# Optimization experiments

Hardware: AMD Instinct MI355X
Metric: run time of the kernel (lower is better)

## Reference

```python
import jax, jax.numpy as jnp
import numpy as np


def setup_inputs() -> dict:
    key = jax.random.key(0)
    ks = jax.random.split(key, 8)
    B, L, D = 8, 4096, 1024
    s = 1.0 / np.sqrt(D)  # torch Linear default init scale (approx)
    return {
        "x": jax.random.normal(ks[0], (B, L, D), dtype=jnp.float32),
        "hidden": jax.random.normal(ks[1], (B, D), dtype=jnp.float32),
        "W_f": jax.random.normal(ks[2], (D, D), dtype=jnp.float32) * s,
        "b_f": jnp.zeros((D,), dtype=jnp.float32),
        "W_i": jax.random.normal(ks[3], (D, D), dtype=jnp.float32) * s,
        "b_i": jnp.zeros((D,), dtype=jnp.float32),
        "W_o": jax.random.normal(ks[4], (D, D), dtype=jnp.float32) * s,
        "b_o": jnp.zeros((D,), dtype=jnp.float32),
    }


def reference(x, hidden, W_f, b_f, W_i, b_i, W_o, b_o):
    # x: [B, L, D], hidden: [B, D]
    D = x.shape[-1]
    lin = jnp.linspace(0.0, 1.0, D, dtype=x.dtype)  # per-channel gate scale
    remember = jax.nn.sigmoid(jnp.einsum('bld,ed->ble', x, W_f) + b_f) * lin
    forget = 1.0 - remember
    inp = jnp.tanh(jnp.einsum('bld,ed->ble', x, W_i) + b_i) * remember

    # linear recurrence h_t = forget_t * h_{t-1} + inp_t  via parallel scan
    def combine(c1, c2):
        a1, u1 = c1
        a2, u2 = c2
        return (a1 * a2, a2 * u1 + u2)

    cumprod_forget, h_inner = jax.lax.associative_scan(combine, (forget, inp), axis=1)
    h = h_inner + hidden[:, None, :] * cumprod_forget  # inject initial hidden state
    y = jnp.einsum('bld,ed->ble', h, W_o) + b_o
    return y, h
```

## Files before the change

### kernel.cpp

```cpp
#include <hip/hip_runtime.h>
#include <stdint.h>

#define B_ 8
#define L_ 4096
#define D_ 1024
#define M_ (B_*L_)
#define CHUNKS 128
#define TCH (L_/CHUNKS)

typedef float f32x4 __attribute__((ext_vector_type(4)));
typedef float f32x2 __attribute__((ext_vector_type(2)));
typedef short short8 __attribute__((ext_vector_type(8)));
typedef unsigned short ushort4v __attribute__((ext_vector_type(4)));

static __device__ __forceinline__ unsigned short f2bf(float f) {
  union { float f; unsigned u; } v; v.f = f;
  unsigned r = v.u + 0x7FFFu + ((v.u >> 16) & 1u);
  return (unsigned short)(r >> 16);
}
static __device__ __forceinline__ float bf2f(unsigned short u) {
  union { unsigned u; float f; } v; v.u = ((unsigned)u) << 16; return v.f;
}

#define GLOAD16(g, l) \
  __builtin_amdgcn_global_load_lds((__attribute__((address_space(1))) const void*)(g), \
                                   (__attribute__((address_space(3))) void*)(l), 16, 0, 0)

__global__ __launch_bounds__(256)
void cvt_bf16(const float* __restrict__ src, unsigned short* __restrict__ dst, int n8)
{
  int gid = blockIdx.x * 256 + threadIdx.x;
  if (gid >= n8) return;
  const f32x4* s = (const f32x4*)(src + (size_t)gid * 8);
  f32x4 v0 = s[0], v1 = s[1];
  union { short8 v; unsigned short u[8]; } w;
  w.u[0] = f2bf(v0[0]); w.u[1] = f2bf(v0[1]); w.u[2] = f2bf(v0[2]); w.u[3] = f2bf(v0[3]);
  w.u[4] = f2bf(v1[0]); w.u[5] = f2bf(v1[1]); w.u[6] = f2bf(v1[2]); w.u[7] = f2bf(v1[3]);
  *(short8*)(dst + (size_t)gid * 8) = w.v;
}

__global__ __launch_bounds__(256)
void cvt_w3(const float* __restrict__ w0, const float* __restrict__ w1,
            const float* __restrict__ w2, unsigned short* __restrict__ dst)
{
  const int per = (D_ * D_) / 8 / 256;
  int m = blockIdx.x / per;
  int gid = (blockIdx.x % per) * 256 + threadIdx.x;
  const float* src = (m == 0) ? w0 : (m == 1) ? w1 : w2;
  const f32x4* s = (const f32x4*)(src + (size_t)gid * 8);
  f32x4 v0 = s[0], v1 = s[1];
  union { short8 v; unsigned short u[8]; } w;
  w.u[0] = f2bf(v0[0]); w.u[1] = f2bf(v0[1]); w.u[2] = f2bf(v0[2]); w.u[3] = f2bf(v0[3]);
  w.u[4] = f2bf(v1[0]); w.u[5] = f2bf(v1[1]); w.u[6] = f2bf(v1[2]); w.u[7] = f2bf(v1[3]);
  *(short8*)(dst + (size_t)m * D_ * D_ + (size_t)gid * 8) = w.v;
}

template<int MODE>
__global__ __launch_bounds__(512, 2)
void gemm256(const unsigned short* __restrict__ A,
             const unsigned short* __restrict__ Bw,
             const float* __restrict__ bias0,
             const float* __restrict__ bias1,
             unsigned short* __restrict__ ob0,
             unsigned short* __restrict__ ob1,
             float* __restrict__ of)
{
  __shared__ unsigned short lds[65536];
  char* ldsb = (char*)lds;

  const int tid  = threadIdx.x;
  const int lane = tid & 63;
  const int wid  = tid >> 6;
  const int wm   = wid >> 2;
  const int wn   = wid & 3;
  const int frow = lane & 15, ks = lane >> 4;
  const int xsw  = (ks ^ ((frow >> 1) & 3)) << 4;

  constexpr int NBN = (MODE == 0) ? 8 : 4;
  constexpr int GBM = 32 / NBN;
  const int xcd   = blockIdx.x & 7;
  const int slot  = blockIdx.x >> 3;
  const int local = slot & 31;
  const int wrnd  = slot >> 5;
  const int bm = (xcd * 16 + wrnd * GBM + (local & (GBM - 1))) * 256;
  const int bn = (local / GBM) * 256;

  const int r0  = tid >> 2;
  const int scl = ((tid & 3) ^ ((r0 >> 1) & 3)) << 4;
  const char* pA = (const char*)A  + (size_t)(bm + r0) * 2048 + scl;
  const char* pB = (const char*)Bw + (size_t)(bn + r0) * 2048 + scl;
  const int dst16 = tid * 16;

  f32x4 acc[8][4] = {};
  short8 aq[4], bq[4];

  auto stgA = [&](int T, int kk, int buf) {
    const char* s = pA + T * 128 + kk * 64;
    char* d = ldsb + buf * 32768 + kk * 16384 + dst16;
    GLOAD16(s, d);
    GLOAD16(s + (size_t)128 * 2048, d + 8192);
  };
  auto stgB = [&](int T, int kk, int buf) {
    const char* s = pB + T * 128 + kk * 64;
    char* d = ldsb + 65536 + buf * 32768 + kk * 16384 + dst16;
    GLOAD16(s, d);
    GLOAD16(s + (size_t)128 * 2048, d + 8192);
  };
  auto ldA4 = [&](const char* LA, int kk, int ih) {
    const char* base = LA + kk * 16384 + (wm * 128 + ih * 64 + frow) * 64 + xsw;
    aq[0] = *(const short8*)(base);
    aq[1] = *(const short8*)(base + 1024);
    aq[2] = *(const short8*)(base + 2048);
    aq[3] = *(const short8*)(base + 3072);
  };
  auto ldB4 = [&](const char* LB, int kk) {
    const char* base = LB + kk * 16384 + (wn * 64 + frow) * 64 + xsw;
    bq[0] = *(const short8*)(base);
    bq[1] = *(const short8*)(base + 1024);
    bq[2] = *(const short8*)(base + 2048);
    bq[3] = *(const short8*)(base + 3072);
  };
  auto mfma16 = [&](int ih) {
    __builtin_amdgcn_s_setprio(1);
    #pragma unroll
    for (int i2 = 0; i2 < 4; ++i2) {
      #pragma unroll
      for (int j = 0; j < 4; ++j)
        acc[ih * 4 + i2][j] =
          __builtin_amdgcn_mfma_f32_16x16x32_bf16(aq[i2], bq[j], acc[ih * 4 + i2][j], 0, 0, 0);
    }
    __builtin_amdgcn_s_setprio(0);
  };

  stgA(0, 0, 0); stgB(0, 0, 0);
  stgA(0, 1, 0); stgB(0, 1, 0);
  stgA(1, 0, 1); stgB(1, 0, 1);
  asm volatile("s_waitcnt vmcnt(8)" ::: "memory");
  __builtin_amdgcn_s_barrier();

  for (int t = 0; t < 16; ++t) {
    const int buf = t & 1;
    const char* LA = ldsb + buf * 32768;
    const char* LB = ldsb + 65536 + buf * 32768;
    ldB4(LB, 0);
    ldA4(LA, 0, 0);
    if (t < 15) stgA(t + 1, 1, (t + 1) & 1);
    __builtin_amdgcn_s_barrier();
    asm volatile("s_waitcnt lgkmcnt(0)" ::: "memory");
    mfma16(0);
    __builtin_amdgcn_s_barrier();
    ldA4(LA, 0, 1);
    if (t < 15) stgB(t + 1, 1, (t + 1) & 1);
    if (t < 15) asm volatile("s_waitcnt vmcnt(8)" ::: "memory");
    else        asm volatile("s_waitcnt vmcnt(0)" ::: "memory");
    __builtin_amdgcn_s_barrier();
    asm volatile("s_waitcnt lgkmcnt(0)" ::: "memory");
    mfma16(1);
    __builtin_amdgcn_s_barrier();
    ldB4(LB, 1);
    ldA4(LA, 1, 0);
    if (t < 14) stgA(t + 2, 0, buf);
    __builtin_amdgcn_s_barrier();
    asm volatile("s_waitcnt lgkmcnt(0)" ::: "memory");
    mfma16(0);
    __builtin_amdgcn_s_barrier();
    ldA4(LA, 1, 1);
    if (t < 14) stgB(t + 2, 0, buf);
    if (t < 14) asm volatile("s_waitcnt vmcnt(8)" ::: "memory");
    else        asm volatile("s_waitcnt vmcnt(4)" ::: "memory");
    __builtin_amdgcn_s_barrier();
    asm volatile("s_waitcnt lgkmcnt(0)" ::: "memory");
    mfma16(1);
    __builtin_amdgcn_s_barrier();
  }

  if constexpr (MODE == 0) {
    const int plane = bn >> 10;
    const int cb    = bn & 1023;
    unsigned short* ob = plane ? ob1 : ob0;
    const float* bs    = plane ? bias1 : bias0;
    float bv[4];
    #pragma unroll
    for (int j = 0; j < 4; ++j) bv[j] = bs[cb + wn * 64 + j * 16 + frow];
    #pragma unroll
    for (int ii = 0; ii < 8; ++ii) {
      int row = bm + wm * 128 + ii * 16 + ks * 4;
      #pragma unroll
      for (int j = 0; j < 4; ++j) {
        int col = cb + wn * 64 + j * 16 + frow;
        #pragma unroll
        for (int r = 0; r < 4; ++r)
          ob[(size_t)(row + r) * D_ + col] = f2bf(acc[ii][j][r] + bv[j]);
      }
    }
  } else {
    float bv[4];
    #pragma unroll
    for (int j = 0; j < 4; ++j) bv[j] = bias0[bn + wn * 64 + j * 16 + frow];
    #pragma unroll
    for (int ii = 0; ii < 8; ++ii) {
      int row = bm + wm * 128 + ii * 16 + ks * 4;
      #pragma unroll
      for (int j = 0; j < 4; ++j) {
        int col = bn + wn * 64 + j * 16 + frow;
        #pragma unroll
        for (int r = 0; r < 4; ++r)
          of[(size_t)(row + r) * D_ + col] = acc[ii][j][r] + bv[j];
      }
    }
  }
}

static __device__ __forceinline__ void gate1(float zf, float zi, float lin,
                                             float& f, float& inp)
{
  float rem = lin / (1.0f + __expf(-zf));
  float ez  = __expf(2.0f * zi);
  float th  = 1.0f - 2.0f / (ez + 1.0f);
  f = 1.0f - rem;
  inp = th * rem;
}

__global__ __launch_bounds__(256)
void scan_partial_b(const unsigned short* __restrict__ zf,
                    const unsigned short* __restrict__ zi,
                    float* __restrict__ Ag, float* __restrict__ Ug)
{
  int blk = blockIdx.x;
  int b = blk >> 7, c = blk & (CHUNKS - 1);
  int e = threadIdx.x << 2;
  float lin0 = (float)e * (1.0f / 1023.0f);
  size_t base = ((size_t)b * L_ + (size_t)c * TCH) * D_ + e;
  f32x4 a = {1.f,1.f,1.f,1.f}, u = {0.f,0.f,0.f,0.f};
  for (int t = 0; t < TCH; ++t) {
    ushort4v f4 = *(const ushort4v*)(zf + base + (size_t)t * D_);
    ushort4v i4 = *(const ushort4v*)(zi + base + (size_t)t * D_);
    #pragma unroll
    for (int j = 0; j < 4; ++j) {
      float fg, inp;
      gate1(bf2f(f4[j]), bf2f(i4[j]), lin0 + (float)j * (1.0f/1023.0f), fg, inp);
      u[j] = fmaf(fg, u[j], inp);
      a[j] *= fg;
    }
  }
  size_t o = (size_t)(b * CHUNKS + c) * D_ + e;
  *(f32x4*)(Ag + o) = a;
  *(f32x4*)(Ug + o) = u;
}

__global__ __launch_bounds__(256)
void scan_carry(const float* __restrict__ Ag, const float* __restrict__ Ug,
                const float* __restrict__ hidden, float* __restrict__ Hin)
{
  int gid = blockIdx.x * 256 + threadIdx.x;
  int b = gid >> 8;
  int e = (gid & 255) << 2;
  f32x4 h = *(const f32x4*)(hidden + (size_t)b * D_ + e);
  for (int c = 0; c < CHUNKS; ++c) {
    size_t o = (size_t)(b * CHUNKS + c) * D_ + e;
    *(f32x4*)(Hin + o) = h;
    f32x4 A = *(const f32x4*)(Ag + o);
    f32x4 U = *(const f32x4*)(Ug + o);
    h = A * h + U;
  }
}

__global__ __launch_bounds__(256)
void scan_apply_b(const unsigned short* __restrict__ zf,
                  const unsigned short* __restrict__ zi,
                  const float* __restrict__ Hin,
                  float* __restrict__ hout, unsigned short* __restrict__ hb)
{
  int blk = blockIdx.x;
  int b = blk >> 7, c = blk & (CHUNKS - 1);
  int e = threadIdx.x << 2;
  float lin0 = (float)e * (1.0f / 1023.0f);
  size_t base = ((size_t)b * L_ + (size_t)c * TCH) * D_ + e;
  f32x4 h = *(const f32x4*)(Hin + (size_t)(b * CHUNKS + c) * D_ + e);
  for (int t = 0; t < TCH; ++t) {
    size_t o = base + (size_t)t * D_;
    ushort4v f4 = *(const ushort4v*)(zf + o);
    ushort4v i4 = *(const ushort4v*)(zi + o);
    #pragma unroll
    for (int j = 0; j < 4; ++j) {
      float fg, inp;
      gate1(bf2f(f4[j]), bf2f(i4[j]), lin0 + (float)j * (1.0f/1023.0f), fg, inp);
      h[j] = fmaf(fg, h[j], inp);
    }
    *(f32x4*)(hout + o) = h;
    ushort4v p;
    p[0] = f2bf(h[0]); p[1] = f2bf(h[1]); p[2] = f2bf(h[2]); p[3] = f2bf(h[3]);
    *(ushort4v*)(hb + o) = p;
  }
}

template<int MODE>
__global__ __launch_bounds__(256, 2)
void gemm_slow(const float* __restrict__ A, const float* __restrict__ B0,
               const float* __restrict__ B1, const float* __restrict__ bias0,
               const float* __restrict__ bias1, float* __restrict__ out0,
               float* __restrict__ out1)
{
  constexpr int BK = 32;
  __shared__ unsigned short As[128 * BK];
  __shared__ unsigned short Bs0[128 * BK];
  __shared__ unsigned short Bs1[(MODE == 0) ? (128 * BK) : 8];

  const int tid = threadIdx.x, lane = tid & 63, wave = tid >> 6;
  const int wr = wave >> 1, wc = wave & 1;
  const int bm = blockIdx.x * 128, bn = blockIdx.y * 128;
  f32x4 acc0[4][4] = {};
  f32x4 acc1[(MODE == 0) ? 4 : 1][(MODE == 0) ? 4 : 1] = {};
  const int frow = lane & 15, kslot = lane >> 4;
  const int xs = kslot ^ (frow & 3);

  auto stage = [&](const float* src, unsigned short* dst) {
    #pragma unroll
    for (int p = 0; p < 4; ++p) {
      int g = p * 256 + tid;
      int row = g >> 3, kq = (g & 7) << 2;
      f32x4 v = *(const f32x4*)(src + (size_t)row * D_ + kq);
      ushort4v w;
      w[0] = f2bf(v[0]); w[1] = f2bf(v[1]); w[2] = f2bf(v[2]); w[3] = f2bf(v[3]);
      int byte = kq << 1, slot = byte >> 4, sub = byte & 15;
      int off = row * 64 + ((slot ^ (row & 3)) << 4) + sub;
      *(ushort4v*)((char*)dst + off) = w;
    }
  };

  for (int k0 = 0; k0 < D_; k0 += BK) {
    stage(A + (size_t)bm * D_ + k0, As);
    stage(B0 + (size_t)bn * D_ + k0, Bs0);
    if constexpr (MODE == 0) stage(B1 + (size_t)bn * D_ + k0, Bs1);
    __syncthreads();
    short8 af[4], bf0[4], bf1[4];
    #pragma unroll
    for (int i = 0; i < 4; ++i) {
      int ar = wr * 64 + i * 16 + frow;
      af[i] = *(const short8*)((const char*)As + ar * 64 + (xs << 4));
      int br = wc * 64 + i * 16 + frow;
      bf0[i] = *(const short8*)((const char*)Bs0 + br * 64 + (xs << 4));
      if constexpr (MODE == 0)
        bf1[i] = *(const short8*)((const char*)Bs1 + br * 64 + (xs << 4));
    }
    #pragma unroll
    for (int i = 0; i < 4; ++i)
      #pragma unroll
      for (int j = 0; j < 4; ++j) {
        acc0[i][j] = __builtin_amdgcn_mfma_f32_16x16x32_bf16(af[i], bf0[j], acc0[i][j], 0, 0, 0);
        if constexpr (MODE == 0)
          acc1[i][j] = __builtin_amdgcn_mfma_f32_16x16x32_bf16(af[i], bf1[j], acc1[i][j], 0, 0, 0);
      }
    __syncthreads();
  }
  #pragma unroll
  for (int i = 0; i < 4; ++i)
    #pragma unroll
    for (int j = 0; j < 4; ++j)
      #pragma unroll
      for (int r = 0; r < 4; ++r) {
        int row = bm + wr * 64 + i * 16 + (lane >> 4) * 4 + r;
        int col = bn + wc * 64 + j * 16 + (lane & 15);
        size_t idx = (size_t)row * D_ + col;
        if constexpr (MODE == 0) {
          float zf = acc0[i][j][r] + bias0[col];
          float linv = (float)col * (1.0f / 1023.0f);
          float rem = linv / (1.0f + __expf(-zf));
          float zi = acc1[i][j][r] + bias1[col];
          float e2 = __expf(2.0f * zi);
          float th = 1.0f - 2.0f / (e2 + 1.0f);
          out0[idx] = 1.0f - rem;
          out1[idx] = th * rem;
        } else {
          out0[idx] = acc0[i][j][r] + bias0[col];
        }
      }
}

__global__ __launch_bounds__(256)
void scan_partial_f(const float* __restrict__ p0, const float* __restrict__ p1,
                    float* __restrict__ Ag, float* __restrict__ Ug)
{
  int blk = blockIdx.x;
  int b = blk / (CHUNKS * 2);
  int c = (blk >> 1) & (CHUNKS - 1);
  int e = ((blk & 1) << 9) + threadIdx.x * 2;
  size_t base = ((size_t)b * L_ + (size_t)c * TCH) * D_ + e;
  f32x2 a = {1.0f, 1.0f}, u = {0.0f, 0.0f};
  for (int t = 0; t < TCH; ++t) {
    f32x2 f = *(const f32x2*)(p0 + base + (size_t)t * D_);
    f32x2 i = *(const f32x2*)(p1 + base + (size_t)t * D_);
    u = f * u + i;
    a = a * f;
  }
  size_t o = (size_t)(b * CHUNKS + c) * D_ + e;
  *(f32x2*)(Ag + o) = a;
  *(f32x2*)(Ug + o) = u;
}

__global__ __launch_bounds__(256)
void scan_apply_f(const float* __restrict__ p0, float* __restrict__ p1_io,
                  const float* __restrict__ Hin)
{
  int blk = blockIdx.x;
  int b = blk / (CHUNKS * 2);
  int c = (blk >> 1) & (CHUNKS - 1);
  int e = ((blk & 1) << 9) + threadIdx.x * 2;
  size_t base = ((size_t)b * L_ + (size_t)c * TCH) * D_ + e;
  f32x2 h = *(const f32x2*)(Hin + (size_t)(b * CHUNKS + c) * D_ + e);
  for (int t = 0; t < TCH; ++t) {
    size_t o = base + (size_t)t * D_;
    f32x2 f = *(const f32x2*)(p0 + o);
    f32x2 i = *(const f32x2*)(p1_io + o);
    h = f * h + i;
    *(f32x2*)(p1_io + o) = h;
  }
}

extern "C" void kernel_launch(void* const* d_in, const int* in_sizes, int n_in,
                              void* d_out, int out_size, void* d_ws, size_t ws_size,
                              hipStream_t stream)
{
  const float* x      = (const float*)d_in[0];
  const float* hidden = (const float*)d_in[1];
  const float* W_f    = (const float*)d_in[2];
  const float* b_f    = (const float*)d_in[3];
  const float* W_i    = (const float*)d_in[4];
  const float* b_i    = (const float*)d_in[5];
  const float* W_o    = (const float*)d_in[6];
  const float* b_o    = (const float*)d_in[7];

  float* y = (float*)d_out;
  float* h = y + (size_t)M_ * D_;

  const size_t xb_elems = (size_t)M_ * D_;
  const size_t w_elems  = (size_t)D_ * D_;
  const size_t agg      = (size_t)B_ * CHUNKS * D_;
  const size_t need = (xb_elems * 3 + 3 * w_elems) * 2 + agg * 3 * 4;

  if (ws_size >= need) {
    unsigned short* xb  = (unsigned short*)d_ws;
    unsigned short* wfb = xb + xb_elems;
    unsigned short* wib = wfb + w_elems;
    unsigned short* wob = wib + w_elems;
    unsigned short* zfb = wob + w_elems;
    unsigned short* zib = zfb + xb_elems;
    float* Ag  = (float*)(zib + xb_elems);
    float* Ug  = Ag + agg;
    float* Hin = Ug + agg;

    cvt_bf16<<<(int)(xb_elems / 8 / 256), 256, 0, stream>>>(x, xb, (int)(xb_elems / 8));
    cvt_w3<<<3 * (int)(w_elems / 8 / 256), 256, 0, stream>>>(W_f, W_i, W_o, wfb);

    gemm256<0><<<1024, 512, 0, stream>>>(xb, wfb, b_f, b_i, zfb, zib, nullptr);

    int pblocks = B_ * CHUNKS;
    scan_partial_b<<<pblocks, 256, 0, stream>>>(zfb, zib, Ag, Ug);
    scan_carry<<<(B_ * D_ / 4) / 256, 256, 0, stream>>>(Ag, Ug, hidden, Hin);
    scan_apply_b<<<pblocks, 256, 0, stream>>>(zfb, zib, Hin, h, xb);

    gemm256<1><<<512, 512, 0, stream>>>(xb, wob, b_o, nullptr, nullptr, nullptr, y);
  } else {
    float* Ag  = (float*)d_ws;
    float* Ug  = Ag + agg;
    float* Hin = Ug + agg;
    dim3 gg(M_ / 128, D_ / 128);
    int pblocks = B_ * CHUNKS * 2;

    gemm_slow<0><<<gg, 256, 0, stream>>>(x, W_f, W_i, b_f, b_i, y, h);
    scan_partial_f<<<pblocks, 256, 0, stream>>>(y, h, Ag, Ug);
    scan_carry<<<(B_ * D_ / 4) / 256, 256, 0, stream>>>(Ag, Ug, hidden, Hin);
    scan_apply_f<<<pblocks, 256, 0, stream>>>(y, h, Hin);
    gemm_slow<1><<<gg, 256, 0, stream>>>(h, W_o, nullptr, b_o, nullptr, y, nullptr);
  }
}
```

Measured before the change: 390.9 us.

## Fuse gate activations into GEMM epilogue and hand-unroll pipelined K loop

```diff
diff --git a/kernel.cpp b/kernel.cpp
--- a/kernel.cpp
+++ b/kernel.cpp
@@ -106,19 +106,24 @@
     GLOAD16(s, d);
     GLOAD16(s + (size_t)128 * 2048, d + 8192);
   };
+  auto ldAB4 = [&](const char* LA, const char* LB, int kk, int ih) {
+    const char* ab = LA + kk * 16384 + (wm * 128 + ih * 64 + frow) * 64 + xsw;
+    const char* bb = LB + kk * 16384 + (wn * 64 + frow) * 64 + xsw;
+    aq[0] = *(const short8*)(ab);
+    bq[0] = *(const short8*)(bb);
+    bq[1] = *(const short8*)(bb + 1024);
+    bq[2] = *(const short8*)(bb + 2048);
+    bq[3] = *(const short8*)(bb + 3072);
+    aq[1] = *(const short8*)(ab + 1024);
+    aq[2] = *(const short8*)(ab + 2048);
+    aq[3] = *(const short8*)(ab + 3072);
+  };
   auto ldA4 = [&](const char* LA, int kk, int ih) {
-    const char* base = LA + kk * 16384 + (wm * 128 + ih * 64 + frow) * 64 + xsw;
-    aq[0] = *(const short8*)(base);
-    aq[1] = *(const short8*)(base + 1024);
-    aq[2] = *(const short8*)(base + 2048);
-    aq[3] = *(const short8*)(base + 3072);
-  };
-  auto ldB4 = [&](const char* LB, int kk) {
-    const char* base = LB + kk * 16384 + (wn * 64 + frow) * 64 + xsw;
-    bq[0] = *(const short8*)(base);
-    bq[1] = *(const short8*)(base + 1024);
-    bq[2] = *(const short8*)(base + 2048);
-    bq[3] = *(const short8*)(base + 3072);
+    const char* ab = LA + kk * 16384 + (wm * 128 + ih * 64 + frow) * 64 + xsw;
+    aq[0] = *(const short8*)(ab);
+    aq[1] = *(const short8*)(ab + 1024);
+    aq[2] = *(const short8*)(ab + 2048);
+    aq[3] = *(const short8*)(ab + 3072);
   };
   auto mfma16 = [&](int ih) {
     __builtin_amdgcn_s_setprio(1);
@@ -132,47 +137,48 @@
     __builtin_amdgcn_s_setprio(0);
   };
 
+#define DO_TILE(T, BUF, STG1, STG2, W1, W3)                                   \
+  {                                                                           \
+    const char* LA = ldsb + (BUF) * 32768;                                    \
+    const char* LB = ldsb + 65536 + (BUF) * 32768;                            \
+    ldAB4(LA, LB, 0, 0);                                                      \
+    if (STG1) stgA((T) + 1, 1, ((T) + 1) & 1);                                \
+    __builtin_amdgcn_s_barrier();                                             \
+    mfma16(0);                                                                \
+    __builtin_amdgcn_s_barrier();                                             \
+    ldA4(LA, 0, 1);                                                           \
+    if (STG1) stgB((T) + 1, 1, ((T) + 1) & 1);                                \
+    asm volatile("s_waitcnt vmcnt(" #W1 ")" ::: "memory");                    \
+    __builtin_amdgcn_s_barrier();                                             \
+    mfma16(1);                                                                \
+    __builtin_amdgcn_s_barrier();                                             \
+    ldAB4(LA, LB, 1, 0);                                                      \
+    if (STG2) stgA((T) + 2, 0, (BUF));                                        \
+    __builtin_amdgcn_s_barrier();                                             \
+    mfma16(0);                                                                \
+    __builtin_amdgcn_s_barrier();                                             \
+    ldA4(LA, 1, 1);                                                           \
+    if (STG2) stgB((T) + 2, 0, (BUF));                                        \
+    asm volatile("s_waitcnt vmcnt(" #W3 ")" ::: "memory");                    \
+    __builtin_amdgcn_s_barrier();                                             \
+    mfma16(1);                                                                \
+    __builtin_amdgcn_s_barrier();                                             \
+  }
+
   stgA(0, 0, 0); stgB(0, 0, 0);
   stgA(0, 1, 0); stgB(0, 1, 0);
   stgA(1, 0, 1); stgB(1, 0, 1);
   asm volatile("s_waitcnt vmcnt(8)" ::: "memory");
   __builtin_amdgcn_s_barrier();
 
-  for (int t = 0; t < 16; ++t) {
-    const int buf = t & 1;
-    const char* LA = ldsb + buf * 32768;
-    const char* LB = ldsb + 65536 + buf * 32768;
-    ldB4(LB, 0);
-    ldA4(LA, 0, 0);
-    if (t < 15) stgA(t + 1, 1, (t + 1) & 1);
-    __builtin_amdgcn_s_barrier();
-    asm volatile("s_waitcnt lgkmcnt(0)" ::: "memory");
-    mfma16(0);
-    __builtin_amdgcn_s_barrier();
-    ldA4(LA, 0, 1);
-    if (t < 15) stgB(t + 1, 1, (t + 1) & 1);
-    if (t < 15) asm volatile("s_waitcnt vmcnt(8)" ::: "memory");
-    else        asm volatile("s_waitcnt vmcnt(0)" ::: "memory");
-    __builtin_amdgcn_s_barrier();
-    asm volatile("s_waitcnt lgkmcnt(0)" ::: "memory");
-    mfma16(1);
-    __builtin_amdgcn_s_barrier();
-    ldB4(LB, 1);
-    ldA4(LA, 1, 0);
-    if (t < 14) stgA(t + 2, 0, buf);
-    __builtin_amdgcn_s_barrier();
-    asm volatile("s_waitcnt lgkmcnt(0)" ::: "memory");
-    mfma16(0);
-    __builtin_amdgcn_s_barrier();
-    ldA4(LA, 1, 1);
-    if (t < 14) stgB(t + 2, 0, buf);
-    if (t < 14) asm volatile("s_waitcnt vmcnt(8)" ::: "memory");
-    else        asm volatile("s_waitcnt vmcnt(4)" ::: "memory");
-    __builtin_amdgcn_s_barrier();
-    asm volatile("s_waitcnt lgkmcnt(0)" ::: "memory");
-    mfma16(1);
-    __builtin_amdgcn_s_barrier();
-  }
+  for (int tt = 0; tt < 7; ++tt) {
+    int t0 = tt * 2;
+    DO_TILE(t0,     0, true, true, 8, 8);
+    DO_TILE(t0 + 1, 1, true, true, 8, 8);
+  }
+  DO_TILE(14, 0, true,  false, 8, 4);
+  DO_TILE(15, 1, false, false, 0, 0);
+#undef DO_TILE
 
   if constexpr (MODE == 0) {
     const int plane = bn >> 10;
@@ -188,9 +194,19 @@
       #pragma unroll
       for (int j = 0; j < 4; ++j) {
         int col = cb + wn * 64 + j * 16 + frow;
+        float lin = (float)col * (1.0f / 1023.0f);
         #pragma unroll
-        for (int r = 0; r < 4; ++r)
-          ob[(size_t)(row + r) * D_ + col] = f2bf(acc[ii][j][r] + bv[j]);
+        for (int r = 0; r < 4; ++r) {
+          float z = acc[ii][j][r] + bv[j];
+          float v;
+          if (plane == 0) {
+            v = lin / (1.0f + __expf(-z));
+          } else {
+            float e2 = __expf(2.0f * z);
+            v = 1.0f - 2.0f / (e2 + 1.0f);
+          }
+          ob[(size_t)(row + r) * D_ + col] = f2bf(v);
+        }
       }
     }
   } else {
@@ -211,36 +227,26 @@
   }
 }
 
-static __device__ __forceinline__ void gate1(float zf, float zi, float lin,
-                                             float& f, float& inp)
-{
-  float rem = lin / (1.0f + __expf(-zf));
-  float ez  = __expf(2.0f * zi);
-  float th  = 1.0f - 2.0f / (ez + 1.0f);
-  f = 1.0f - rem;
-  inp = th * rem;
-}
-
-__global__ __launch_bounds__(256)
-void scan_partial_b(const unsigned short* __restrict__ zf,
-                    const unsigned short* __restrict__ zi,
+__global__ __launch_bounds__(256)
+void scan_partial_b(const unsigned short* __restrict__ rb,
+                    const unsigned short* __restrict__ tb,
                     float* __restrict__ Ag, float* __restrict__ Ug)
 {
   int blk = blockIdx.x;
   int b = blk >> 7, c = blk & (CHUNKS - 1);
   int e = threadIdx.x << 2;
-  float lin0 = (float)e * (1.0f / 1023.0f);
   size_t base = ((size_t)b * L_ + (size_t)c * TCH) * D_ + e;
   f32x4 a = {1.f,1.f,1.f,1.f}, u = {0.f,0.f,0.f,0.f};
   for (int t = 0; t < TCH; ++t) {
-    ushort4v f4 = *(const ushort4v*)(zf + base + (size_t)t * D_);
-    ushort4v i4 = *(const ushort4v*)(zi + base + (size_t)t * D_);
+    ushort4v r4 = *(const ushort4v*)(rb + base + (size_t)t * D_);
+    ushort4v t4 = *(const ushort4v*)(tb + base + (size_t)t * D_);
     #pragma unroll
     for (int j = 0; j < 4; ++j) {
-      float fg, inp;
-      gate1(bf2f(f4[j]), bf2f(i4[j]), lin0 + (float)j * (1.0f/1023.0f), fg, inp);
-      u[j] = fmaf(fg, u[j], inp);
-      a[j] *= fg;
+      float rem = bf2f(r4[j]);
+      float f   = 1.0f - rem;
+      float inp = bf2f(t4[j]) * rem;
+      u[j] = fmaf(f, u[j], inp);
+      a[j] *= f;
     }
   }
   size_t o = (size_t)(b * CHUNKS + c) * D_ + e;
@@ -266,26 +272,26 @@
 }
 
 __global__ __launch_bounds__(256)
-void scan_apply_b(const unsigned short* __restrict__ zf,
-                  const unsigned short* __restrict__ zi,
+void scan_apply_b(const unsigned short* __restrict__ rb,
+                  const unsigned short* __restrict__ tb,
                   const float* __restrict__ Hin,
                   float* __restrict__ hout, unsigned short* __restrict__ hb)
 {
   int blk = blockIdx.x;
   int b = blk >> 7, c = blk & (CHUNKS - 1);
   int e = threadIdx.x << 2;
-  float lin0 = (float)e * (1.0f / 1023.0f);
   size_t base = ((size_t)b * L_ + (size_t)c * TCH) * D_ + e;
   f32x4 h = *(const f32x4*)(Hin + (size_t)(b * CHUNKS + c) * D_ + e);
   for (int t = 0; t < TCH; ++t) {
     size_t o = base + (size_t)t * D_;
-    ushort4v f4 = *(const ushort4v*)(zf + o);
-    ushort4v i4 = *(const ushort4v*)(zi + o);
+    ushort4v r4 = *(const ushort4v*)(rb + o);
+    ushort4v t4 = *(const ushort4v*)(tb + o);
     #pragma unroll
     for (int j = 0; j < 4; ++j) {
-      float fg, inp;
-      gate1(bf2f(f4[j]), bf2f(i4[j]), lin0 + (float)j * (1.0f/1023.0f), fg, inp);
-      h[j] = fmaf(fg, h[j], inp);
+      float rem = bf2f(r4[j]);
+      float f   = 1.0f - rem;
+      float inp = bf2f(t4[j]) * rem;
+      h[j] = fmaf(f, h[j], inp);
     }
     *(f32x4*)(hout + o) = h;
     ushort4v p;
@@ -443,21 +449,21 @@
     unsigned short* wfb = xb + xb_elems;
     unsigned short* wib = wfb + w_elems;
     unsigned short* wob = wib + w_elems;
-    unsigned short* zfb = wob + w_elems;
-    unsigned short* zib = zfb + xb_elems;
-    float* Ag  = (float*)(zib + xb_elems);
+    unsigned short* rbv = wob + w_elems;
+    unsigned short* tbv = rbv + xb_elems;
+    float* Ag  = (float*)(tbv + xb_elems);
     float* Ug  = Ag + agg;
     float* Hin = Ug + agg;
 
     cvt_bf16<<<(int)(xb_elems / 8 / 256), 256, 0, stream>>>(x, xb, (int)(xb_elems / 8));
     cvt_w3<<<3 * (int)(w_elems / 8 / 256), 256, 0, stream>>>(W_f, W_i, W_o, wfb);
 
-    gemm256<0><<<1024, 512, 0, stream>>>(xb, wfb, b_f, b_i, zfb, zib, nullptr);
+    gemm256<0><<<1024, 512, 0, stream>>>(xb, wfb, b_f, b_i, rbv, tbv, nullptr);
 
     int pblocks = B_ * CHUNKS;
-    scan_partial_b<<<pblocks, 256, 0, stream>>>(zfb, zib, Ag, Ug);
+    scan_partial_b<<<pblocks, 256, 0, stream>>>(rbv, tbv, Ag, Ug);
     scan_carry<<<(B_ * D_ / 4) / 256, 256, 0, stream>>>(Ag, Ug, hidden, Hin);
-    scan_apply_b<<<pblocks, 256, 0, stream>>>(zfb, zib, Hin, h, xb);
+    scan_apply_b<<<pblocks, 256, 0, stream>>>(rbv, tbv, Hin, h, xb);
 
     gemm256<1><<<512, 512, 0, stream>>>(xb, wob, b_o, nullptr, nullptr, nullptr, y);
   } else {
```

Result: no change. 388.7 us (-0.6%).
